# Kernel optimization log

Hardware: AMD Instinct MI355X
Metric: run time of the kernel (lower is better)

The kernel has to match this reference:

```python
import jax, jax.numpy as jnp
import numpy as np
import math

B, N, DIN, H, DH, DV, DENC, MAXLEN = 8, 1024, 1024, 8, 128, 64, 32, 1024
EPS = 1e-5


def _make_pe():
    # sinusoidal table, stored as a learnable parameter in the torch module
    pos = np.arange(MAXLEN, dtype=np.float32)[:, None]
    div = np.exp(np.arange(0, DENC, 2, dtype=np.float32) * (-math.log(10000.0) / DENC))
    pe = np.zeros((MAXLEN, DENC), np.float32)
    pe[:, 0::2] = np.sin(pos * div)
    pe[:, 1::2] = np.cos(pos * div)
    return jnp.asarray(pe)[None]  # (1, MAXLEN, DENC)


def setup_inputs() -> dict:
    key = jax.random.key(0)
    ks = jax.random.split(key, 4)
    dq = DH * H  # = d_q = d_k = 1024
    return {
        "x": jax.random.normal(ks[0], (B, N, DIN), jnp.float32),
        "gamma": jnp.ones((1, 1, DIN), jnp.float32),
        "beta": jnp.zeros((1, 1, DIN), jnp.float32),
        "pe": _make_pe(),
        "W_pos": jax.random.normal(ks[1], (DIN + DENC, DIN), jnp.float32) * 0.02,
        "b_pos": jnp.zeros((DIN,), jnp.float32),
        "W_qkv": jax.random.normal(ks[2], (DIN, 2 * dq + DV * H), jnp.float32) * 0.02,
        "b_qkv": jnp.zeros((2 * dq + DV * H,), jnp.float32),
        "W_out": jax.random.normal(ks[3], (DV * H, DIN), jnp.float32) * 0.02,
        "b_out": jnp.zeros((DIN,), jnp.float32),
        "scale": jnp.asarray(1.414, jnp.float32),
    }


def reference(x, gamma, beta, pe, W_pos, b_pos, W_qkv, b_qkv, W_out, b_out, scale):
    Bq, Nq, _ = x.shape
    # PositionalEncoding: concat sinusoidal table, project back to d_in, residual add
    pos_in = jnp.concatenate([x, jnp.broadcast_to(pe[:, :Nq], (Bq, Nq, DENC))], axis=-1)
    h = x + (pos_in @ W_pos + b_pos)
    # FeatureNorm: normalize over the SEQUENCE dim (dim=1), biased variance
    mean = h.mean(axis=1, keepdims=True)
    var = h.var(axis=1, keepdims=True)
    hn = gamma * (h - mean) * jax.lax.rsqrt(var + EPS) + beta
    # QKV projection and head split
    qkv = hn @ W_qkv + b_qkv
    dq = DH * H
    q = qkv[..., :dq].reshape(Bq, Nq, H, DH).transpose(0, 2, 1, 3)       # (B,H,N,DH)
    k = qkv[..., dq:2 * dq].reshape(Bq, Nq, H, DH).transpose(0, 2, 1, 3)  # (B,H,N,DH)
    v = qkv[..., 2 * dq:].reshape(Bq, Nq, H, DV).transpose(0, 2, 1, 3)    # (B,H,N,DV)
    # for_twdit branch: attn = softmax(-(cdist(q,k)/scale)^2) == softmax(-||q-k||^2/scale^2)
    sq = jnp.sum(q * q, axis=-1)  # (B,H,N)
    sk = jnp.sum(k * k, axis=-1)  # (B,H,N)
    d2 = sq[..., :, None] + sk[..., None, :] - 2.0 * jnp.einsum('bhnc,bhmc->bhnm', q, k)
    d2 = jnp.maximum(d2, 0.0)  # cdist is a true (nonnegative) distance
    attn = jax.nn.softmax(-d2 / (scale * scale), axis=-1)  # (B,H,N,N)
    out = jnp.einsum('bhnm,bhmd->bhnd', attn, v)            # (B,H,N,DV)
    out = out.transpose(0, 2, 1, 3).reshape(Bq, Nq, H * DV)
    return x + (out @ W_out + b_out)
```

## Files before the change

### kernel.cpp

```cpp
#include <hip/hip_runtime.h>
#include <math.h>

typedef __bf16 bf16;
typedef __attribute__((ext_vector_type(8))) __bf16 bf16x8;
typedef __attribute__((ext_vector_type(4))) float f32x4;

#define MFMA16(a, b, c) __builtin_amdgcn_mfma_f32_16x16x32_bf16(a, b, c, 0, 0, 0)

__device__ __forceinline__ void gld_lds16(const void* g, void* l) {
  __builtin_amdgcn_global_load_lds(
      (const __attribute__((address_space(1))) unsigned int*)g,
      (__attribute__((address_space(3))) unsigned int*)l, 16, 0, 0);
}

__global__ __launch_bounds__(256) void prep_kernel(
    const float* __restrict__ x, const float* __restrict__ W_pos,
    const float* __restrict__ W_qkv, const float* __restrict__ W_out,
    const float* __restrict__ pe,
    bf16* __restrict__ x_bf, bf16* __restrict__ wpos_t, bf16* __restrict__ wqkv_t,
    bf16* __restrict__ wout_t, bf16* __restrict__ pe_pj) {
  __shared__ float tile[32][33];
  const int tid = threadIdx.x;
  int blk = blockIdx.x;
  if (blk < 4096) {
    int idx = blk * 256 + tid;
    const float4 a = ((const float4*)x)[idx * 2];
    const float4 b = ((const float4*)x)[idx * 2 + 1];
    bf16x8 o = {(bf16)a.x, (bf16)a.y, (bf16)a.z, (bf16)a.w,
                (bf16)b.x, (bf16)b.y, (bf16)b.z, (bf16)b.w};
    *(bf16x8*)(x_bf + (size_t)idx * 8) = o;
    return;
  }
  blk -= 4096;
  if (blk < 4096) {
    const float* W; bf16* WT; int K, N, bx, by;
    if (blk < 1024)      { W = W_pos; WT = wpos_t; K = 1024; N = 1024; bx = blk & 31; by = blk >> 5; }
    else if (blk < 3584) { int b2 = blk - 1024; W = W_qkv; WT = wqkv_t; K = 1024; N = 2560; bx = b2 % 80; by = b2 / 80; }
    else                 { int b2 = blk - 3584; W = W_out; WT = wout_t; K = 512;  N = 1024; bx = b2 & 31; by = b2 >> 5; }
    const int n0 = bx * 32, k0 = by * 32;
    const int tx = tid & 31, ty = tid >> 5;
#pragma unroll
    for (int i = 0; i < 4; ++i)
      tile[ty + 8 * i][tx] = W[(size_t)(k0 + ty + 8 * i) * N + n0 + tx];
    __syncthreads();
#pragma unroll
    for (int i = 0; i < 4; ++i)
      WT[(size_t)(n0 + ty + 8 * i) * K + k0 + tx] = (bf16)tile[tx][ty + 8 * i];
    return;
  }
  blk -= 4096;
  int idx = blk * 256 + tid;
  int n = idx >> 10, c = idx & 1023;
  float s = 0.f;
#pragma unroll
  for (int e = 0; e < 32; ++e)
    s += pe[n * 32 + e] * W_pos[(size_t)(1024 + e) * 1024 + c];
  pe_pj[idx] = (bf16)s;
}

template <int NT, int OUT_BF16>
__global__ __launch_bounds__(512) void gemm_bf16(
    const bf16* __restrict__ A, const bf16* __restrict__ BT, void* __restrict__ Cout,
    int M, int N, int K,
    const float* __restrict__ bias, const bf16* __restrict__ add_full,
    const bf16* __restrict__ add_mod) {
  __shared__ __align__(16) bf16 As[3][128 * 64];
  __shared__ __align__(16) bf16 Bs[3][256 * 64];
  const int tid = threadIdx.x;
  const int wave = tid >> 6, lane = tid & 63;
  const int wr = wave >> 2, wc = wave & 3;
  const int lr = lane & 15, lg = lane >> 4;

  const int nwg = gridDim.x * gridDim.y;
  const int bid = blockIdx.y * gridDim.x + blockIdx.x;
  const int s = (bid & 7) * (nwg >> 3) + (bid >> 3);
  const int row0 = (s / gridDim.x) * 128, col0 = (s % gridDim.x) * 256;

  const int trow = tid >> 3;
  const int cbd = ((tid & 7) * 16) ^ ((trow & 7) << 4);
  const bf16* asrc = A + (size_t)(row0 + trow) * K + (cbd >> 1);
  const bf16* bsrc = BT + (size_t)(col0 + trow) * K + (cbd >> 1);
  f32x4 acc[4][4] = {};

  auto STAGE = [&](int sel, int t) {
    const int kt = t * 64;
    char* al = (char*)&As[sel][0] + tid * 16;
    char* bl = (char*)&Bs[sel][0] + tid * 16;
#pragma unroll
    for (int c = 0; c < 2; ++c)
      gld_lds16(asrc + (size_t)c * 64 * K + kt, al + c * 8192);
#pragma unroll
    for (int c = 0; c < 4; ++c)
      gld_lds16(bsrc + (size_t)c * 64 * K + kt, bl + c * 8192);
  };

  STAGE(0, 0);
  STAGE(1, 1);

#pragma unroll
  for (int t = 0; t < NT; ++t) {
    if (t + 1 < NT)
      asm volatile("s_waitcnt vmcnt(6)" ::: "memory");
    else
      asm volatile("s_waitcnt vmcnt(0)" ::: "memory");
    __builtin_amdgcn_s_barrier();
    if (t + 2 < NT) STAGE((t + 2) % 3, t + 2);
    const char* Ab = (const char*)&As[t % 3][0];
    const char* Bb = (const char*)&Bs[t % 3][0];
#pragma unroll
    for (int kc = 0; kc < 2; ++kc) {
      bf16x8 af[4], bfr[4];
#pragma unroll
      for (int mt = 0; mt < 4; ++mt) {
        int r = wr * 64 + mt * 16 + lr;
        int byte = r * 128 + (((kc * 32 + lg * 8) * 2) ^ ((r & 7) << 4));
        af[mt] = *(const bf16x8*)(Ab + byte);
      }
#pragma unroll
      for (int nt = 0; nt < 4; ++nt) {
        int c = wc * 64 + nt * 16 + lr;
        int byte = c * 128 + (((kc * 32 + lg * 8) * 2) ^ ((c & 7) << 4));
        bfr[nt] = *(const bf16x8*)(Bb + byte);
      }
      __builtin_amdgcn_s_setprio(1);
#pragma unroll
      for (int mt = 0; mt < 4; ++mt)
#pragma unroll
        for (int nt = 0; nt < 4; ++nt)
          acc[mt][nt] = MFMA16(af[mt], bfr[nt], acc[mt][nt]);
      __builtin_amdgcn_s_setprio(0);
    }
  }

#pragma unroll
  for (int mt = 0; mt < 4; ++mt) {
#pragma unroll
    for (int v = 0; v < 4; ++v) {
      int r = row0 + wr * 64 + mt * 16 + lg * 4 + v;
#pragma unroll
      for (int nt = 0; nt < 4; ++nt) {
        int c = col0 + wc * 64 + nt * 16 + lr;
        float val = acc[mt][nt][v];
        if (bias) val += bias[c];
        if (add_full) val += (float)add_full[(size_t)r * N + c];
        if (add_mod) val += (float)add_mod[(size_t)(r & 1023) * N + c];
        if (OUT_BF16)
          ((bf16*)Cout)[(size_t)r * N + c] = (bf16)val;
        else
          ((float*)Cout)[(size_t)r * N + c] = val;
      }
    }
  }
}

__global__ __launch_bounds__(512) void featnorm_kernel(const bf16* __restrict__ h,
                                                       bf16* __restrict__ hn,
                                                       const float* __restrict__ gamma,
                                                       const float* __restrict__ beta) {
  const int b = blockIdx.x >> 4;
  const int d0 = (blockIdx.x & 15) << 6;
  const int tid = threadIdx.x;
  const int c = tid & 63, g = tid >> 6;
  const size_t base = (size_t)b * (1024 * 1024) + d0 + c;
  float s = 0.f, s2 = 0.f;
  for (int n = g * 128; n < g * 128 + 128; ++n) {
    float v = (float)h[base + (size_t)n * 1024];
    s += v; s2 += v * v;
  }
  __shared__ float rs[8][64], rs2[8][64];
  rs[g][c] = s; rs2[g][c] = s2;
  __syncthreads();
  __shared__ float smean[64], srstd[64];
  if (tid < 64) {
    float S = 0.f, S2 = 0.f;
#pragma unroll
    for (int q = 0; q < 8; ++q) { S += rs[q][tid]; S2 += rs2[q][tid]; }
    float mean = S * (1.f / 1024.f);
    float var = S2 * (1.f / 1024.f) - mean * mean;
    smean[tid] = mean;
    srstd[tid] = rsqrtf(var + 1e-5f);
  }
  __syncthreads();
  const float mean = smean[c], rstd = srstd[c];
  const float gm = gamma[d0 + c], bt = beta[d0 + c];
  for (int n = g * 128; n < g * 128 + 128; ++n) {
    size_t idx = base + (size_t)n * 1024;
    hn[idx] = (bf16)(gm * ((float)h[idx] - mean) * rstd + bt);
  }
}

__global__ __launch_bounds__(256) void skvt_kernel(const bf16* __restrict__ qkv,
                                                   const float* __restrict__ scale_ptr,
                                                   float* __restrict__ skl,
                                                   bf16* __restrict__ vT) {
  const int tid = threadIdx.x;
  if (blockIdx.x < 4096) {
    const int lr = tid & 15;
    const int task = blockIdx.x * 16 + (tid >> 4);
    const int bh = task >> 10, n = task & 1023;
    const int b = bh >> 3, h = bh & 7;
    const bf16x8 v = *(const bf16x8*)(qkv + (size_t)(b * 1024 + n) * 2560 +
                                      1024 + h * 128 + lr * 8);
    float s = 0.f;
#pragma unroll
    for (int i = 0; i < 8; ++i) { float f = (float)v[i]; s += f * f; }
#pragma unroll
    for (int off = 1; off < 16; off <<= 1) s += __shfl_xor(s, off);
    if (lr == 0) {
      float sc = scale_ptr[0];
      skl[task] = s * (1.44269504f / (sc * sc));
    }
    return;
  }
  __shared__ bf16 tile[32][34];
  const int blk = blockIdx.x - 4096;
  const int b = blk >> 9;
  const int rem = blk & 511;
  const int c0 = (rem >> 5) * 32, n0 = (rem & 31) * 32;
  const int tx = tid & 31, ty = tid >> 5;
#pragma unroll
  for (int i = 0; i < 4; ++i)
    tile[ty + 8 * i][tx] = qkv[(size_t)(b * 1024 + n0 + ty + 8 * i) * 2560 + 2048 + c0 + tx];
  __syncthreads();
#pragma unroll
  for (int i = 0; i < 4; ++i)
    vT[(size_t)(b * 512 + c0 + ty + 8 * i) * 1024 + n0 + tx] = tile[tx][ty + 8 * i];
}

__global__ __launch_bounds__(512, 4) void attn_mfma(const bf16* __restrict__ qkv,
                                                    const bf16* __restrict__ vT,
                                                    const float* __restrict__ skl,
                                                    const float* __restrict__ scale_ptr,
                                                    bf16* __restrict__ attn_o) {
  const int swz = ((blockIdx.x & 7) << 6) + (blockIdx.x >> 3);
  const int it = swz & 7, bh = swz >> 3;
  const int b = bh >> 3, h = bh & 7;
  const int i0 = it * 128;
  const int tid = threadIdx.x, wave = tid >> 6, lane = tid & 63;
  const int lr = lane & 15, lg = lane >> 4;
  const float sc = scale_ptr[0];
  const float c2 = 2.f * 1.44269504f / (sc * sc);

  __shared__ __align__(16) bf16 Ks[2][64 * 128];
  __shared__ __align__(16) bf16 Vs[2][64 * 64];
  __shared__ __align__(16) bf16 Ps[8][16 * 64];
  __shared__ float sks[1024];

  const int trowK = tid >> 4;
  const int cbKd = ((tid & 15) * 16) ^ ((trowK & 7) << 4);
  const bf16* ksrc = qkv + (size_t)(b * 1024 + trowK) * 2560 + 1024 + h * 128 + (cbKd >> 1);
  const int trowV = tid >> 3;
  const int cbVd = ((tid & 7) * 16) ^ ((trowV & 7) << 4);
  const bf16* vsrc = vT + (size_t)(b * 512 + h * 64 + trowV) * 1024 + (cbVd >> 1);

  auto STAGE = [&](int sel, int jt) {
    const bf16* kp = ksrc + (size_t)jt * 64 * 2560;
    char* kl = (char*)&Ks[sel][0] + tid * 16;
    gld_lds16(kp, kl);
    gld_lds16(kp + (size_t)32 * 2560, kl + 8192);
    gld_lds16(vsrc + jt * 64, (char*)&Vs[sel][0] + tid * 16);
  };

  {
    float2 sv = ((const float2*)(skl + (size_t)bh * 1024))[tid];
    *(float2*)&sks[tid * 2] = sv;
  }
  bf16x8 qf[4];
  {
    const bf16* qrow = qkv + (size_t)(b * 1024 + i0 + wave * 16 + lr) * 2560 + h * 128;
#pragma unroll
    for (int kc = 0; kc < 4; ++kc) qf[kc] = *(const bf16x8*)(qrow + kc * 32 + lg * 8);
  }
  __syncthreads();

  bf16x8 vones;
  {
    bf16 one_or_zero = (lr == 0) ? (bf16)1.0f : (bf16)0.0f;
#pragma unroll
    for (int i = 0; i < 8; ++i) vones[i] = one_or_zero;
  }

  f32x4 o[4] = {};
  f32x4 o_l = {};

  STAGE(0, 0);
  asm volatile("s_waitcnt vmcnt(0)" ::: "memory");
  __builtin_amdgcn_s_barrier();

#pragma unroll
  for (int jt = 0; jt < 16; ++jt) {
    const int cur = jt & 1;
    if (jt < 15) STAGE(cur ^ 1, jt + 1);

    f32x4 sacc[4] = {};
    __builtin_amdgcn_s_setprio(1);
#pragma unroll
    for (int kc = 0; kc < 4; ++kc) {
#pragma unroll
      for (int nt = 0; nt < 4; ++nt) {
        int j = nt * 16 + lr;
        int byte = j * 256 + (((kc * 32 + lg * 8) * 2) ^ ((j & 7) << 4));
        bf16x8 kf = *(const bf16x8*)((const char*)&Ks[cur][0] + byte);
        sacc[nt] = MFMA16(qf[kc], kf, sacc[nt]);
      }
    }
    __builtin_amdgcn_s_setprio(0);

#pragma unroll
    for (int nt = 0; nt < 4; ++nt) {
      float skv = sks[jt * 64 + nt * 16 + lr];
#pragma unroll
      for (int v = 0; v < 4; ++v) {
        float p = __builtin_amdgcn_exp2f(sacc[nt][v] * c2 - skv);
        int r = lg * 4 + v, c = nt * 16 + lr;
        int byte = r * 128 + ((c * 2) ^ ((r & 7) << 4));
        *(bf16*)((char*)&Ps[wave][0] + byte) = (bf16)p;
      }
    }
    bf16x8 pf[2];
#pragma unroll
    for (int kc = 0; kc < 2; ++kc) {
      int byte = lr * 128 + (((kc * 32 + lg * 8) * 2) ^ ((lr & 7) << 4));
      pf[kc] = *(const bf16x8*)((const char*)&Ps[wave][0] + byte);
    }
    __builtin_amdgcn_s_setprio(1);
#pragma unroll
    for (int kc = 0; kc < 2; ++kc) {
#pragma unroll
      for (int nt = 0; nt < 4; ++nt) {
        int d = nt * 16 + lr;
        int byte = d * 128 + (((kc * 32 + lg * 8) * 2) ^ ((d & 7) << 4));
        bf16x8 vf = *(const bf16x8*)((const char*)&Vs[cur][0] + byte);
        o[nt] = MFMA16(pf[kc], vf, o[nt]);
      }
      o_l = MFMA16(pf[kc], vones, o_l);
    }
    __builtin_amdgcn_s_setprio(0);

    asm volatile("s_waitcnt vmcnt(0)" ::: "memory");
    __builtin_amdgcn_s_barrier();
  }

#pragma unroll
  for (int v = 0; v < 4; ++v) {
    float ls = __shfl(o_l[v], lg << 4);
    float inv = 1.f / ls;
    int r = i0 + wave * 16 + lg * 4 + v;
#pragma unroll
    for (int nt = 0; nt < 4; ++nt) {
      int c = h * 64 + nt * 16 + lr;
      attn_o[(size_t)(b * 1024 + r) * 512 + c] = (bf16)(o[nt][v] * inv);
    }
  }
}

extern "C" void kernel_launch(void* const* d_in, const int* in_sizes, int n_in,
                              void* d_out, int out_size, void* d_ws, size_t ws_size,
                              hipStream_t stream) {
  const float* x     = (const float*)d_in[0];
  const float* gamma = (const float*)d_in[1];
  const float* beta  = (const float*)d_in[2];
  const float* pe    = (const float*)d_in[3];
  const float* W_pos = (const float*)d_in[4];
  const float* b_pos = (const float*)d_in[5];
  const float* W_qkv = (const float*)d_in[6];
  const float* b_qkv = (const float*)d_in[7];
  const float* W_out = (const float*)d_in[8];
  const float* b_out = (const float*)d_in[9];
  const float* scale = (const float*)d_in[10];
  float* outp = (float*)d_out;

  char* ws = (char*)d_ws;
  const size_t MB = 1 << 20;
  bf16* x_bf   = (bf16*)(ws);
  bf16* wpos_t = (bf16*)(ws + 16 * MB);
  bf16* wqkv_t = (bf16*)(ws + 18 * MB);
  bf16* wout_t = (bf16*)(ws + 23 * MB);
  bf16* pe_pj  = (bf16*)(ws + 24 * MB);
  bf16* vT     = (bf16*)(ws + 24 * MB);
  bf16* h      = (bf16*)(ws + 32 * MB);
  bf16* attn_o = (bf16*)(ws + 32 * MB);
  bf16* qkv    = (bf16*)(ws + 48 * MB);
  float* skl   = (float*)(ws + 88 * MB);
  bf16* hn     = (bf16*)(ws + 96 * MB);

  prep_kernel<<<12288, 256, 0, stream>>>(x, W_pos, W_qkv, W_out, pe,
                                         x_bf, wpos_t, wqkv_t, wout_t, pe_pj);
  gemm_bf16<16, 1><<<dim3(4, 64), 512, 0, stream>>>(x_bf, wpos_t, h, 8192, 1024, 1024,
                                                    b_pos, x_bf, pe_pj);
  featnorm_kernel<<<128, 512, 0, stream>>>(h, hn, gamma, beta);
  gemm_bf16<16, 1><<<dim3(10, 64), 512, 0, stream>>>(hn, wqkv_t, qkv, 8192, 2560, 1024,
                                                     b_qkv, nullptr, nullptr);
  skvt_kernel<<<8192, 256, 0, stream>>>(qkv, scale, skl, vT);
  attn_mfma<<<512, 512, 0, stream>>>(qkv, vT, skl, scale, attn_o);
  gemm_bf16<8, 0><<<dim3(4, 64), 512, 0, stream>>>(attn_o, wout_t, outp, 8192, 1024, 512,
                                                   b_out, x_bf, nullptr);
}
```

Baseline: 252.9 us.

## Pre-pack weights into MFMA fragment layout and load B directly from global

The weight preprocessing now writes each weight matrix in a blocked layout that matches the MFMA B-fragment, 16 columns by 8 k-values per 16-byte chunk. The GEMM then reads B fragments straight from global memory into registers instead of staging them through LDS. This removes the large B LDS buffers and their barrier traffic, cuts LDS use, and lets a launch bound of 4 blocks per CU allow more occupancy. The pipeline is also reordered so the wait and barrier come after compute. The cost is that B fragments are re-read from global or L2 by every wave row, with latency that is not hidden by async staging.

```diff
diff --git a/kernel.cpp b/kernel.cpp
--- a/kernel.cpp
+++ b/kernel.cpp
@@ -17,8 +17,8 @@
     const float* __restrict__ x, const float* __restrict__ W_pos,
     const float* __restrict__ W_qkv, const float* __restrict__ W_out,
     const float* __restrict__ pe,
-    bf16* __restrict__ x_bf, bf16* __restrict__ wpos_t, bf16* __restrict__ wqkv_t,
-    bf16* __restrict__ wout_t, bf16* __restrict__ pe_pj) {
+    bf16* __restrict__ x_bf, bf16* __restrict__ wpos_p, bf16* __restrict__ wqkv_p,
+    bf16* __restrict__ wout_p, bf16* __restrict__ pe_pj) {
   __shared__ float tile[32][33];
   const int tid = threadIdx.x;
   int blk = blockIdx.x;
@@ -33,19 +33,24 @@
   }
   blk -= 4096;
   if (blk < 4096) {
-    const float* W; bf16* WT; int K, N, bx, by;
-    if (blk < 1024)      { W = W_pos; WT = wpos_t; K = 1024; N = 1024; bx = blk & 31; by = blk >> 5; }
-    else if (blk < 3584) { int b2 = blk - 1024; W = W_qkv; WT = wqkv_t; K = 1024; N = 2560; bx = b2 % 80; by = b2 / 80; }
-    else                 { int b2 = blk - 3584; W = W_out; WT = wout_t; K = 512;  N = 1024; bx = b2 & 31; by = b2 >> 5; }
+    const float* W; bf16* BP; int K, N, bx, by;
+    if (blk < 1024)      { W = W_pos; BP = wpos_p; K = 1024; N = 1024; bx = blk & 31; by = blk >> 5; }
+    else if (blk < 3584) { int b2 = blk - 1024; W = W_qkv; BP = wqkv_p; K = 1024; N = 2560; bx = b2 % 80; by = b2 / 80; }
+    else                 { int b2 = blk - 3584; W = W_out; BP = wout_p; K = 512;  N = 1024; bx = b2 & 31; by = b2 >> 5; }
     const int n0 = bx * 32, k0 = by * 32;
     const int tx = tid & 31, ty = tid >> 5;
 #pragma unroll
     for (int i = 0; i < 4; ++i)
       tile[ty + 8 * i][tx] = W[(size_t)(k0 + ty + 8 * i) * N + n0 + tx];
     __syncthreads();
-#pragma unroll
-    for (int i = 0; i < 4; ++i)
-      WT[(size_t)(n0 + ty + 8 * i) * K + k0 + tx] = (bf16)tile[tx][ty + 8 * i];
+    if (tid < 128) {
+      int cc = tid & 31, kq = tid >> 5;
+      int c = n0 + cc, k = k0 + kq * 8;
+      bf16x8 v;
+#pragma unroll
+      for (int i = 0; i < 8; ++i) v[i] = (bf16)tile[kq * 8 + i][cc];
+      *(bf16x8*)(BP + ((size_t)(c >> 4) * (K >> 3) + (k >> 3)) * 128 + (c & 15) * 8) = v;
+    }
     return;
   }
   blk -= 4096;
@@ -59,77 +64,69 @@
 }
 
 template <int NT, int OUT_BF16>
-__global__ __launch_bounds__(512) void gemm_bf16(
-    const bf16* __restrict__ A, const bf16* __restrict__ BT, void* __restrict__ Cout,
+__global__ __launch_bounds__(512, 4) void gemm_bd(
+    const bf16* __restrict__ A, const bf16* __restrict__ BP, void* __restrict__ Cout,
     int M, int N, int K,
     const float* __restrict__ bias, const bf16* __restrict__ add_full,
     const bf16* __restrict__ add_mod) {
   __shared__ __align__(16) bf16 As[3][128 * 64];
-  __shared__ __align__(16) bf16 Bs[3][256 * 64];
   const int tid = threadIdx.x;
   const int wave = tid >> 6, lane = tid & 63;
   const int wr = wave >> 2, wc = wave & 3;
   const int lr = lane & 15, lg = lane >> 4;
+  const int KB = K >> 3;
 
   const int nwg = gridDim.x * gridDim.y;
   const int bid = blockIdx.y * gridDim.x + blockIdx.x;
   const int s = (bid & 7) * (nwg >> 3) + (bid >> 3);
   const int row0 = (s / gridDim.x) * 128, col0 = (s % gridDim.x) * 256;
+  const int cb0 = (col0 >> 4) + wc * 4;
 
   const int trow = tid >> 3;
   const int cbd = ((tid & 7) * 16) ^ ((trow & 7) << 4);
   const bf16* asrc = A + (size_t)(row0 + trow) * K + (cbd >> 1);
-  const bf16* bsrc = BT + (size_t)(col0 + trow) * K + (cbd >> 1);
   f32x4 acc[4][4] = {};
 
   auto STAGE = [&](int sel, int t) {
-    const int kt = t * 64;
     char* al = (char*)&As[sel][0] + tid * 16;
-    char* bl = (char*)&Bs[sel][0] + tid * 16;
-#pragma unroll
-    for (int c = 0; c < 2; ++c)
-      gld_lds16(asrc + (size_t)c * 64 * K + kt, al + c * 8192);
-#pragma unroll
-    for (int c = 0; c < 4; ++c)
-      gld_lds16(bsrc + (size_t)c * 64 * K + kt, bl + c * 8192);
+    gld_lds16(asrc + t * 64, al);
+    gld_lds16(asrc + (size_t)64 * K + t * 64, al + 8192);
   };
 
   STAGE(0, 0);
   STAGE(1, 1);
+  asm volatile("s_waitcnt vmcnt(2)" ::: "memory");
+  __builtin_amdgcn_s_barrier();
 
 #pragma unroll
   for (int t = 0; t < NT; ++t) {
-    if (t + 1 < NT)
-      asm volatile("s_waitcnt vmcnt(6)" ::: "memory");
+    if (t + 2 < NT) STAGE((t + 2) % 3, t + 2);
+    const char* Ab = (const char*)&As[t % 3][0];
+#pragma unroll
+    for (int kc = 0; kc < 2; ++kc) {
+      const int kb = (t << 3) + kc * 4 + lg;
+      bf16x8 bfr[4], af[4];
+#pragma unroll
+      for (int nt = 0; nt < 4; ++nt)
+        bfr[nt] = *(const bf16x8*)(BP + ((size_t)(cb0 + nt) * KB + kb) * 128 + lr * 8);
+#pragma unroll
+      for (int mt = 0; mt < 4; ++mt) {
+        int r = wr * 64 + mt * 16 + lr;
+        af[mt] = *(const bf16x8*)(Ab + r * 128 + ((kc * 64 + lg * 16) ^ ((r & 7) << 4)));
+      }
+      __builtin_amdgcn_s_setprio(1);
+#pragma unroll
+      for (int mt = 0; mt < 4; ++mt)
+#pragma unroll
+        for (int nt = 0; nt < 4; ++nt)
+          acc[mt][nt] = MFMA16(af[mt], bfr[nt], acc[mt][nt]);
+      __builtin_amdgcn_s_setprio(0);
+    }
+    if (t + 2 < NT)
+      asm volatile("s_waitcnt vmcnt(2)" ::: "memory");
     else
       asm volatile("s_waitcnt vmcnt(0)" ::: "memory");
     __builtin_amdgcn_s_barrier();
-    if (t + 2 < NT) STAGE((t + 2) % 3, t + 2);
-    const char* Ab = (const char*)&As[t % 3][0];
-    const char* Bb = (const char*)&Bs[t % 3][0];
-#pragma unroll
-    for (int kc = 0; kc < 2; ++kc) {
-      bf16x8 af[4], bfr[4];
-#pragma unroll
-      for (int mt = 0; mt < 4; ++mt) {
-        int r = wr * 64 + mt * 16 + lr;
-        int byte = r * 128 + (((kc * 32 + lg * 8) * 2) ^ ((r & 7) << 4));
-        af[mt] = *(const bf16x8*)(Ab + byte);
-      }
-#pragma unroll
-      for (int nt = 0; nt < 4; ++nt) {
-        int c = wc * 64 + nt * 16 + lr;
-        int byte = c * 128 + (((kc * 32 + lg * 8) * 2) ^ ((c & 7) << 4));
-        bfr[nt] = *(const bf16x8*)(Bb + byte);
-      }
-      __builtin_amdgcn_s_setprio(1);
-#pragma unroll
-      for (int mt = 0; mt < 4; ++mt)
-#pragma unroll
-        for (int nt = 0; nt < 4; ++nt)
-          acc[mt][nt] = MFMA16(af[mt], bfr[nt], acc[mt][nt]);
-      __builtin_amdgcn_s_setprio(0);
-    }
   }
 
 #pragma unroll
@@ -373,9 +370,9 @@
   char* ws = (char*)d_ws;
   const size_t MB = 1 << 20;
   bf16* x_bf   = (bf16*)(ws);
-  bf16* wpos_t = (bf16*)(ws + 16 * MB);
-  bf16* wqkv_t = (bf16*)(ws + 18 * MB);
-  bf16* wout_t = (bf16*)(ws + 23 * MB);
+  bf16* wpos_p = (bf16*)(ws + 16 * MB);
+  bf16* wqkv_p = (bf16*)(ws + 18 * MB);
+  bf16* wout_p = (bf16*)(ws + 23 * MB);
   bf16* pe_pj  = (bf16*)(ws + 24 * MB);
   bf16* vT     = (bf16*)(ws + 24 * MB);
   bf16* h      = (bf16*)(ws + 32 * MB);
@@ -385,14 +382,14 @@
   bf16* hn     = (bf16*)(ws + 96 * MB);
 
   prep_kernel<<<12288, 256, 0, stream>>>(x, W_pos, W_qkv, W_out, pe,
-                                         x_bf, wpos_t, wqkv_t, wout_t, pe_pj);
-  gemm_bf16<16, 1><<<dim3(4, 64), 512, 0, stream>>>(x_bf, wpos_t, h, 8192, 1024, 1024,
-                                                    b_pos, x_bf, pe_pj);
+                                         x_bf, wpos_p, wqkv_p, wout_p, pe_pj);
+  gemm_bd<16, 1><<<dim3(4, 64), 512, 0, stream>>>(x_bf, wpos_p, h, 8192, 1024, 1024,
+                                                  b_pos, x_bf, pe_pj);
   featnorm_kernel<<<128, 512, 0, stream>>>(h, hn, gamma, beta);
-  gemm_bf16<16, 1><<<dim3(10, 64), 512, 0, stream>>>(hn, wqkv_t, qkv, 8192, 2560, 1024,
-                                                     b_qkv, nullptr, nullptr);
+  gemm_bd<16, 1><<<dim3(10, 64), 512, 0, stream>>>(hn, wqkv_p, qkv, 8192, 2560, 1024,
+                                                   b_qkv, nullptr, nullptr);
   skvt_kernel<<<8192, 256, 0, stream>>>(qkv, scale, skl, vT);
   attn_mfma<<<512, 512, 0, stream>>>(qkv, vT, skl, scale, attn_o);
-  gemm_bf16<8, 0><<<dim3(4, 64), 512, 0, stream>>>(attn_o, wout_t, outp, 8192, 1024, 512,
-                                                   b_out, x_bf, nullptr);
-}
+  gemm_bd<8, 0><<<dim3(4, 64), 512, 0, stream>>>(attn_o, wout_p, outp, 8192, 1024, 512,
+                                                 b_out, x_bf, nullptr);
+}
```

Result: faster. 246.3 us (-2.6%).
